# Kernel optimization log

Measured on AMD Instinct MI355X. Metric: run time of the kernel, lower is better.

Reference implementation:

```python
import jax, jax.numpy as jnp
import numpy as np

N = 50000      # nodes
E = 800000     # directed edges
D = 128        # input_dim == hidden_dim
EL = 100000    # edges scored by decoder


def setup_inputs() -> dict:
    key = jax.random.key(0)
    ks = jax.random.split(key, 8)
    s = 1.0 / np.sqrt(D)  # glorot-ish scale
    return {
        "node_feature": jax.random.normal(ks[0], (N, D), jnp.float32),
        "W1": jax.random.normal(ks[1], (D, D), jnp.float32) * s,
        "b1": jnp.zeros((D,), jnp.float32),
        "W2": jax.random.normal(ks[2], (D, D), jnp.float32) * s,
        "b2": jnp.zeros((D,), jnp.float32),
        "W3": jax.random.normal(ks[3], (D, D), jnp.float32) * s,
        "b3": jnp.zeros((D,), jnp.float32),
        "edge_index": jax.random.randint(ks[4], (2, E), 0, N, dtype=jnp.int32),
        "edge_label_index": jax.random.randint(ks[5], (2, EL), 0, N, dtype=jnp.int32),
    }


def _gcn_conv(x, W, b, src, dst, norm, n):
    # x' = D^{-1/2} (A + I) D^{-1/2} (x W) + b   (PyG GCNConv semantics)
    h = x @ W                                   # [N, D]
    msg = h[src] * norm[:, None]                # gather + scale, [E+N, D]
    out = jax.ops.segment_sum(msg, dst, num_segments=n)  # scatter-add
    return out + b


def reference(node_feature, W1, b1, W2, b2, W3, b3, edge_index, edge_label_index):
    n = node_feature.shape[0]
    loop = jnp.arange(n, dtype=edge_index.dtype)
    src = jnp.concatenate([edge_index[0], loop])  # self-loops appended
    dst = jnp.concatenate([edge_index[1], loop])
    # symmetric normalization: deg over destinations (incl. self-loops)
    deg = jax.ops.segment_sum(jnp.ones_like(dst, dtype=node_feature.dtype), dst, num_segments=n)
    dinv = jax.lax.rsqrt(jnp.maximum(deg, 1.0))
    norm = dinv[src] * dinv[dst]                 # [E+N]

    x = jax.nn.relu(_gcn_conv(node_feature, W1, b1, src, dst, norm, n))
    x = jax.nn.relu(_gcn_conv(x, W2, b2, src, dst, norm, n))
    x = _gcn_conv(x, W3, b3, src, dst, norm, n)

    # dot-product edge decoder
    u = x[edge_label_index[0]]
    v = x[edge_label_index[1]]
    return jnp.sum(u * v, axis=-1)               # [EL] logits
```

## Files before the change

kernel.cpp:

```cpp
#include <hip/hip_runtime.h>
#include <hip/hip_bf16.h>
#include <hip/hip_fp16.h>

typedef _Float16 v8h __attribute__((ext_vector_type(8)));
typedef _Float16 v4h __attribute__((ext_vector_type(4)));
typedef float v4f __attribute__((ext_vector_type(4)));

__global__ __launch_bounds__(256) void wswz(const float* __restrict__ W1,
                                            const float* __restrict__ W2,
                                            const float* __restrict__ W3,
                                            __half* __restrict__ wfrag) {
    int o = blockIdx.x * 256 + threadIdx.x;
    int w = o >> 14, r = o & 16383;
    const float* Ws = (w >= 3) ? W3 : ((w == 2) ? W2 : W1);
    float v = Ws[r];
    __half h;
    if (w == 1) {
        __half hv = __float2half_rn(v);
        h = __float2half_rn(v - __half2float(hv));
    } else {
        h = __float2half_rn(v);
    }
    int k = r >> 7, ncol = r & 127;
    int c = ncol >> 4, nl = ncol & 15;
    int s = k >> 5, quad = (k >> 3) & 3, j = k & 7;
    int di = ((c * 4 + s) * 64 + quad * 16 + nl) * 8 + j;
    wfrag[(size_t)w * 16384 + di] = h;
}

__global__ __launch_bounds__(256) void gemm1_mfma(const float* __restrict__ X,
                                                  const __half* __restrict__ wfrag,
                                                  __half* __restrict__ H, int Nrows,
                                                  int degBlocks,
                                                  const int* __restrict__ dst,
                                                  int* __restrict__ cnt,
                                                  int* __restrict__ rank, int E) {
    int tid = threadIdx.x;
    if (blockIdx.x < degBlocks) {
        int base = blockIdx.x * 2048 + tid * 8;
        if (base + 7 < E) {
            int4 d0 = *(const int4*)&dst[base];
            int4 d1 = *(const int4*)&dst[base + 4];
            int r0 = atomicAdd(&cnt[d0.x * 16], 1);
            int r1 = atomicAdd(&cnt[d0.y * 16], 1);
            int r2 = atomicAdd(&cnt[d0.z * 16], 1);
            int r3 = atomicAdd(&cnt[d0.w * 16], 1);
            int r4 = atomicAdd(&cnt[d1.x * 16], 1);
            int r5 = atomicAdd(&cnt[d1.y * 16], 1);
            int r6 = atomicAdd(&cnt[d1.z * 16], 1);
            int r7 = atomicAdd(&cnt[d1.w * 16], 1);
            *(int4*)&rank[base]     = make_int4(r0, r1, r2, r3);
            *(int4*)&rank[base + 4] = make_int4(r4, r5, r6, r7);
        } else {
            for (int e = base; e < E; ++e) rank[e] = atomicAdd(&cnt[dst[e] * 16], 1);
        }
        return;
    }
    int gb = blockIdx.x - degBlocks;
    int rowbase = gb * 64;
    int l = tid & 63;
    int wid = tid >> 6;
    int rb = wid * 16;
    int quad = l >> 4;
    int nn = l & 15;
    int gr = rowbase + rb + nn;
    v8h ah[4], al[4];
    if (gr < Nrows) {
        const float* Xr = &X[(size_t)gr * 128 + quad * 8];
#pragma unroll
        for (int k = 0; k < 4; ++k) {
            float4 f0 = *(const float4*)&Xr[k * 32];
            float4 f1 = *(const float4*)&Xr[k * 32 + 4];
            float ff[8] = {f0.x, f0.y, f0.z, f0.w, f1.x, f1.y, f1.z, f1.w};
            v8h h, lo;
#pragma unroll
            for (int m = 0; m < 8; ++m) {
                _Float16 hv = (_Float16)ff[m];
                h[m] = hv;
                lo[m] = (_Float16)(ff[m] - (float)hv);
            }
            ah[k] = h;
            al[k] = lo;
        }
    } else {
#pragma unroll
        for (int k = 0; k < 4; ++k) {
            v8h z;
#pragma unroll
            for (int m = 0; m < 8; ++m) z[m] = (_Float16)0.f;
            ah[k] = z;
            al[k] = z;
        }
    }
    const v8h* Wh = (const v8h*)wfrag;
    const v8h* Wl = (const v8h*)(wfrag + 16384);
    v4f acc[8] = {};
#pragma unroll
    for (int c = 0; c < 8; ++c) {
        v8h bh0 = Wh[(c * 4 + 0) * 64 + l];
        v8h bh1 = Wh[(c * 4 + 1) * 64 + l];
        v8h bh2 = Wh[(c * 4 + 2) * 64 + l];
        v8h bh3 = Wh[(c * 4 + 3) * 64 + l];
        acc[c] = __builtin_amdgcn_mfma_f32_16x16x32_f16(ah[0], bh0, acc[c], 0, 0, 0);
        acc[c] = __builtin_amdgcn_mfma_f32_16x16x32_f16(ah[1], bh1, acc[c], 0, 0, 0);
        acc[c] = __builtin_amdgcn_mfma_f32_16x16x32_f16(ah[2], bh2, acc[c], 0, 0, 0);
        acc[c] = __builtin_amdgcn_mfma_f32_16x16x32_f16(ah[3], bh3, acc[c], 0, 0, 0);
        acc[c] = __builtin_amdgcn_mfma_f32_16x16x32_f16(al[0], bh0, acc[c], 0, 0, 0);
        acc[c] = __builtin_amdgcn_mfma_f32_16x16x32_f16(al[1], bh1, acc[c], 0, 0, 0);
        acc[c] = __builtin_amdgcn_mfma_f32_16x16x32_f16(al[2], bh2, acc[c], 0, 0, 0);
        acc[c] = __builtin_amdgcn_mfma_f32_16x16x32_f16(al[3], bh3, acc[c], 0, 0, 0);
        v8h bl0 = Wl[(c * 4 + 0) * 64 + l];
        v8h bl1 = Wl[(c * 4 + 1) * 64 + l];
        v8h bl2 = Wl[(c * 4 + 2) * 64 + l];
        v8h bl3 = Wl[(c * 4 + 3) * 64 + l];
        acc[c] = __builtin_amdgcn_mfma_f32_16x16x32_f16(ah[0], bl0, acc[c], 0, 0, 0);
        acc[c] = __builtin_amdgcn_mfma_f32_16x16x32_f16(ah[1], bl1, acc[c], 0, 0, 0);
        acc[c] = __builtin_amdgcn_mfma_f32_16x16x32_f16(ah[2], bl2, acc[c], 0, 0, 0);
        acc[c] = __builtin_amdgcn_mfma_f32_16x16x32_f16(ah[3], bl3, acc[c], 0, 0, 0);
    }
#pragma unroll
    for (int reg = 0; reg < 4; ++reg) {
        int grr = rowbase + rb + quad * 4 + reg;
        if (grr < Nrows) {
#pragma unroll
            for (int c = 0; c < 8; ++c)
                H[(size_t)grr * 128 + c * 16 + nn] = __float2half_rn(acc[c][reg]);
        }
    }
}

__global__ __launch_bounds__(256) void agg_gemm(const __half* __restrict__ Xs,
                                                const float* __restrict__ dinv,
                                                const int* __restrict__ rowptr,
                                                const int* __restrict__ col,
                                                const __half* __restrict__ wfrag,
                                                const float* __restrict__ bias,
                                                __half* __restrict__ Out,
                                                int n, int finalLayer) {
    __shared__ __align__(16) _Float16 y[64][136];
    int tid = threadIdx.x;
    int rowbase = blockIdx.x * 64;
    {
        int sub = tid >> 4;
        int t = (tid & 15) * 8;
        for (int g = 0; g < 4; ++g) {
            int rr = g * 16 + sub;
            int node = rowbase + rr;
            float a[8] = {};
            if (node < n) {
                int beg = rowptr[node], end = rowptr[node + 1];
                int k = beg;
                for (; k + 4 <= end; k += 4) {
                    int s0 = col[k], s1 = col[k + 1], s2 = col[k + 2], s3 = col[k + 3];
                    uint4 r0 = *(const uint4*)&Xs[(size_t)s0 * 128 + t];
                    uint4 r1 = *(const uint4*)&Xs[(size_t)s1 * 128 + t];
                    uint4 r2 = *(const uint4*)&Xs[(size_t)s2 * 128 + t];
                    uint4 r3 = *(const uint4*)&Xs[(size_t)s3 * 128 + t];
                    const __half2* h0 = (const __half2*)&r0;
                    const __half2* h1 = (const __half2*)&r1;
                    const __half2* h2 = (const __half2*)&r2;
                    const __half2* h3 = (const __half2*)&r3;
#pragma unroll
                    for (int m = 0; m < 4; ++m) {
                        float2 f0 = __half22float2(h0[m]);
                        float2 f1 = __half22float2(h1[m]);
                        float2 f2 = __half22float2(h2[m]);
                        float2 f3 = __half22float2(h3[m]);
                        a[2 * m]     += (f0.x + f1.x) + (f2.x + f3.x);
                        a[2 * m + 1] += (f0.y + f1.y) + (f2.y + f3.y);
                    }
                }
                for (; k < end; ++k) {
                    uint4 r0 = *(const uint4*)&Xs[(size_t)col[k] * 128 + t];
                    const __half2* h0 = (const __half2*)&r0;
#pragma unroll
                    for (int m = 0; m < 4; ++m) {
                        float2 f0 = __half22float2(h0[m]);
                        a[2 * m] += f0.x;
                        a[2 * m + 1] += f0.y;
                    }
                }
                float dn = dinv[node];
#pragma unroll
                for (int m = 0; m < 8; ++m) a[m] *= dn;
            }
            v8h yv;
#pragma unroll
            for (int m = 0; m < 8; ++m) yv[m] = (_Float16)a[m];
            *(v8h*)&y[rr][t] = yv;
        }
    }
    __syncthreads();
    int l = tid & 63;
    int wid = tid >> 6;
    int rb = wid * 16;
    int quad = l >> 4;
    int nn = l & 15;
    v8h a0 = *(const v8h*)&y[rb + nn][0 * 32 + quad * 8];
    v8h a1 = *(const v8h*)&y[rb + nn][1 * 32 + quad * 8];
    v8h a2 = *(const v8h*)&y[rb + nn][2 * 32 + quad * 8];
    v8h a3 = *(const v8h*)&y[rb + nn][3 * 32 + quad * 8];
    const v8h* Wf = (const v8h*)wfrag;
    v4f acc[8] = {};
#pragma unroll
    for (int c = 0; c < 8; ++c) {
        v8h b0 = Wf[(c * 4 + 0) * 64 + l];
        v8h b1 = Wf[(c * 4 + 1) * 64 + l];
        v8h b2 = Wf[(c * 4 + 2) * 64 + l];
        v8h b3 = Wf[(c * 4 + 3) * 64 + l];
        acc[c] = __builtin_amdgcn_mfma_f32_16x16x32_f16(a0, b0, acc[c], 0, 0, 0);
        acc[c] = __builtin_amdgcn_mfma_f32_16x16x32_f16(a1, b1, acc[c], 0, 0, 0);
        acc[c] = __builtin_amdgcn_mfma_f32_16x16x32_f16(a2, b2, acc[c], 0, 0, 0);
        acc[c] = __builtin_amdgcn_mfma_f32_16x16x32_f16(a3, b3, acc[c], 0, 0, 0);
    }
#pragma unroll
    for (int reg = 0; reg < 4; ++reg) {
        int gr = rowbase + rb + quad * 4 + reg;
        if (gr < n) {
            float dn = dinv[gr];
#pragma unroll
            for (int c = 0; c < 8; ++c) {
                float z = acc[c][reg] + bias[c * 16 + nn];
                if (!finalLayer) z = fmaxf(z, 0.f) * dn;
                Out[(size_t)gr * 128 + c * 16 + nn] = __float2half_rn(z);
            }
        }
    }
}

__global__ void scanA(const int* __restrict__ cnt, int* __restrict__ tmp,
                      int* __restrict__ bsum, int n) {
    __shared__ int s[256];
    int i = blockIdx.x * 256 + threadIdx.x;
    int v = (i < n) ? (cnt[i * 16] + 1) : 0;
    s[threadIdx.x] = v;
    __syncthreads();
    for (int off = 1; off < 256; off <<= 1) {
        int x = (threadIdx.x >= off) ? s[threadIdx.x - off] : 0;
        __syncthreads();
        s[threadIdx.x] += x;
        __syncthreads();
    }
    if (i < n) tmp[i] = s[threadIdx.x];
    if (threadIdx.x == 255) bsum[blockIdx.x] = s[255];
}

__global__ void scanB(const int* __restrict__ tmp, const int* __restrict__ bsum,
                      const int* __restrict__ cnt, int* __restrict__ rowptr,
                      float* __restrict__ dinv, int* __restrict__ col, int n, int nb) {
    __shared__ int p[256];
    int t = threadIdx.x;
    p[t] = (t < nb) ? bsum[t] : 0;
    __syncthreads();
    for (int off = 1; off < 256; off <<= 1) {
        int x = (t >= off) ? p[t - off] : 0;
        __syncthreads();
        p[t] += x;
        __syncthreads();
    }
    int prefix = (blockIdx.x == 0) ? 0 : p[blockIdx.x - 1];
    int i = blockIdx.x * 256 + t;
    if (i < n) {
        int inc = tmp[i] + prefix;
        rowptr[i + 1] = inc;
        int c1 = cnt[i * 16] + 1;
        dinv[i] = rsqrtf((float)c1);
        col[inc - c1] = i;
        if (i == 0) rowptr[0] = 0;
    }
}

__global__ __launch_bounds__(256) void fill4(const int* __restrict__ src,
                                             const int* __restrict__ dst,
                                             const int* __restrict__ rank,
                                             const int* __restrict__ rowptr,
                                             int* __restrict__ col, int E) {
    int base = blockIdx.x * 1024 + threadIdx.x * 4;
    if (base + 3 < E) {
        int d0 = dst[base], d1 = dst[base + 1], d2 = dst[base + 2], d3 = dst[base + 3];
        int s0 = src[base], s1 = src[base + 1], s2 = src[base + 2], s3 = src[base + 3];
        int r0 = rank[base], r1 = rank[base + 1], r2 = rank[base + 2], r3 = rank[base + 3];
        col[rowptr[d0] + 1 + r0] = s0;
        col[rowptr[d1] + 1 + r1] = s1;
        col[rowptr[d2] + 1 + r2] = s2;
        col[rowptr[d3] + 1 + r3] = s3;
    } else {
        for (int e = base; e < E; ++e)
            col[rowptr[dst[e]] + 1 + rank[e]] = src[e];
    }
}

__global__ __launch_bounds__(256) void agg_h(const __half* __restrict__ H,
                                             const float* __restrict__ dinv,
                                             const int* __restrict__ rowptr,
                                             const int* __restrict__ col,
                                             const float* __restrict__ bias,
                                             __half* __restrict__ out, int n) {
    int node = blockIdx.x * 16 + (threadIdx.x >> 4);
    int t = (threadIdx.x & 15) * 8;
    if (node >= n) return;
    int beg = rowptr[node], end = rowptr[node + 1];
    float a[8] = {};
    int k = beg;
    for (; k + 4 <= end; k += 4) {
        int s0 = col[k], s1 = col[k + 1], s2 = col[k + 2], s3 = col[k + 3];
        float w0 = dinv[s0], w1 = dinv[s1], w2 = dinv[s2], w3 = dinv[s3];
        uint4 r0 = *(const uint4*)&H[(size_t)s0 * 128 + t];
        uint4 r1 = *(const uint4*)&H[(size_t)s1 * 128 + t];
        uint4 r2 = *(const uint4*)&H[(size_t)s2 * 128 + t];
        uint4 r3 = *(const uint4*)&H[(size_t)s3 * 128 + t];
        const __half2* h0 = (const __half2*)&r0;
        const __half2* h1 = (const __half2*)&r1;
        const __half2* h2 = (const __half2*)&r2;
        const __half2* h3 = (const __half2*)&r3;
#pragma unroll
        for (int m = 0; m < 4; ++m) {
            float2 f0 = __half22float2(h0[m]);
            float2 f1 = __half22float2(h1[m]);
            float2 f2 = __half22float2(h2[m]);
            float2 f3 = __half22float2(h3[m]);
            a[2 * m]     += f0.x * w0 + f1.x * w1 + f2.x * w2 + f3.x * w3;
            a[2 * m + 1] += f0.y * w0 + f1.y * w1 + f2.y * w2 + f3.y * w3;
        }
    }
    for (; k < end; ++k) {
        int s0 = col[k];
        float w0 = dinv[s0];
        uint4 r0 = *(const uint4*)&H[(size_t)s0 * 128 + t];
        const __half2* h0 = (const __half2*)&r0;
#pragma unroll
        for (int m = 0; m < 4; ++m) {
            float2 f0 = __half22float2(h0[m]);
            a[2 * m] += f0.x * w0;
            a[2 * m + 1] += f0.y * w0;
        }
    }
    float dn = dinv[node];
    float4 b0 = *(const float4*)&bias[t];
    float4 b1 = *(const float4*)&bias[t + 4];
    float r0 = fmaxf(a[0] * dn + b0.x, 0.f) * dn;
    float r1 = fmaxf(a[1] * dn + b0.y, 0.f) * dn;
    float r2 = fmaxf(a[2] * dn + b0.z, 0.f) * dn;
    float r3 = fmaxf(a[3] * dn + b0.w, 0.f) * dn;
    float r4 = fmaxf(a[4] * dn + b1.x, 0.f) * dn;
    float r5 = fmaxf(a[5] * dn + b1.y, 0.f) * dn;
    float r6 = fmaxf(a[6] * dn + b1.z, 0.f) * dn;
    float r7 = fmaxf(a[7] * dn + b1.w, 0.f) * dn;
    auto pk = [](float x, float y) { __half2 h = __floats2half2_rn(x, y); return *(unsigned int*)&h; };
    uint4 o = make_uint4(pk(r0, r1), pk(r2, r3), pk(r4, r5), pk(r6, r7));
    *(uint4*)&out[(size_t)node * 128 + t] = o;
}

__global__ __launch_bounds__(256) void decoder_h(const __half* __restrict__ X,
                                                 const int* __restrict__ eli,
                                                 float* __restrict__ out, int EL) {
    int e = blockIdx.x * 16 + (threadIdx.x >> 4);
    int lane = threadIdx.x & 15;
    if (e >= EL) return;
    int u = eli[e], v = eli[EL + e];
    uint4 ra = *(const uint4*)&X[(size_t)u * 128 + lane * 8];
    uint4 rb = *(const uint4*)&X[(size_t)v * 128 + lane * 8];
    const __half2* ha = (const __half2*)&ra;
    const __half2* hb = (const __half2*)&rb;
    float d = 0.f;
#pragma unroll
    for (int j = 0; j < 4; ++j) {
        float2 fa = __half22float2(ha[j]);
        float2 fb = __half22float2(hb[j]);
        d += fa.x * fb.x + fa.y * fb.y;
    }
#pragma unroll
    for (int off = 8; off > 0; off >>= 1) d += __shfl_xor(d, off);
    if (lane == 0) out[e] = d;
}

extern "C" void kernel_launch(void* const* d_in, const int* in_sizes, int n_in,
                              void* d_out, int out_size, void* d_ws, size_t ws_size,
                              hipStream_t stream) {
    const float* x0 = (const float*)d_in[0];
    const float* W1 = (const float*)d_in[1];
    const float* b1 = (const float*)d_in[2];
    const float* W2 = (const float*)d_in[3];
    const float* b2 = (const float*)d_in[4];
    const float* W3 = (const float*)d_in[5];
    const float* b3 = (const float*)d_in[6];
    const int* ei   = (const int*)d_in[7];
    const int* eli  = (const int*)d_in[8];
    float* out = (float*)d_out;

    const int D = 128;
    const int N  = in_sizes[0] / D;
    const int E  = in_sizes[7] / 2;
    const int EL = in_sizes[8] / 2;

    const int* src = ei;
    const int* dst = ei + E;

    char* ws = (char*)d_ws;
    size_t off = 0;
    auto alloc = [&](size_t bytes) -> void* {
        off = (off + 255) & ~(size_t)255;
        void* p = ws + off;
        off += bytes;
        return p;
    };
    int*    cnt    = (int*)alloc((size_t)N * 16 * sizeof(int));
    int*    tmp    = (int*)alloc((size_t)N * sizeof(int));
    int*    bsum   = (int*)alloc(256 * sizeof(int));
    int*    rowptr = (int*)alloc((size_t)(N + 1) * sizeof(int));
    float*  dinv   = (float*)alloc((size_t)N * sizeof(float));
    int*    rank   = (int*)alloc((size_t)E * sizeof(int));
    int*    col    = (int*)alloc((size_t)(E + N) * sizeof(int));
    __half* wfrag  = (__half*)alloc((size_t)4 * 16384 * sizeof(__half));
    __half* hbuf   = (__half*)alloc((size_t)N * D * sizeof(__half));
    __half* xbuf   = (__half*)alloc((size_t)N * D * sizeof(__half));
    (void)ws_size;

    hipMemsetAsync(cnt, 0, (size_t)N * 16 * sizeof(int), stream);

    int nbN = (N + 255) / 256;
    int nbE4 = (E + 1023) / 1024;
    int nbE8 = (E + 2047) / 2048;
    int gemmGrid = (N + 63) / 64;
    int fusedGrid = (N + 63) / 64;
    int aggGrid  = (N + 15) / 16;

    wswz<<<256, 256, 0, stream>>>(W1, W2, W3, wfrag);

    gemm1_mfma<<<nbE8 + gemmGrid, 256, 0, stream>>>(x0, wfrag, hbuf, N,
                                                    nbE8, dst, cnt, rank, E);

    scanA<<<nbN, 256, 0, stream>>>(cnt, tmp, bsum, N);
    scanB<<<nbN, 256, 0, stream>>>(tmp, bsum, cnt, rowptr, dinv, col, N, nbN);
    fill4<<<nbE4, 256, 0, stream>>>(src, dst, rank, rowptr, col, E);

    agg_h<<<aggGrid, 256, 0, stream>>>(hbuf, dinv, rowptr, col, b1, xbuf, N);
    agg_gemm<<<fusedGrid, 256, 0, stream>>>(xbuf, dinv, rowptr, col, wfrag + 2 * 16384, b2, hbuf, N, 0);
    agg_gemm<<<fusedGrid, 256, 0, stream>>>(hbuf, dinv, rowptr, col, wfrag + 3 * 16384, b3, xbuf, N, 1);

    decoder_h<<<(EL + 15) / 16, 256, 0, stream>>>(xbuf, eli, out, EL);
}
```

Baseline: 266.5 us.

## Split degree counting from GEMM, compact counters, unroll gathers by eight

The fused degree-count/GEMM launch is split into a standalone deg_rank kernel and a plain gemm1 kernel. The degree counter array drops its 16-int padding, so the memset and scan reads shrink. gemm1 prefetches the next high-part weight fragments while the low-part MFMAs run, and the aggregation loops gain an 8-wide unrolled gather to keep more loads in flight. The risks are losing the overlap between atomics and GEMM that the fused launch gave, and more atomic contention on densely packed counters.

```diff
diff --git a/kernel.cpp b/kernel.cpp
--- a/kernel.cpp
+++ b/kernel.cpp
@@ -28,36 +28,27 @@
     wfrag[(size_t)w * 16384 + di] = h;
 }
 
-__global__ __launch_bounds__(256) void gemm1_mfma(const float* __restrict__ X,
-                                                  const __half* __restrict__ wfrag,
-                                                  __half* __restrict__ H, int Nrows,
-                                                  int degBlocks,
-                                                  const int* __restrict__ dst,
-                                                  int* __restrict__ cnt,
-                                                  int* __restrict__ rank, int E) {
+__global__ __launch_bounds__(256) void deg_rank(const int* __restrict__ dst,
+                                                int* __restrict__ cnt,
+                                                int* __restrict__ rank, int E) {
+    int base = blockIdx.x * 1024 + threadIdx.x * 4;
+    if (base + 3 < E) {
+        int4 d = *(const int4*)&dst[base];
+        int r0 = atomicAdd(&cnt[d.x], 1);
+        int r1 = atomicAdd(&cnt[d.y], 1);
+        int r2 = atomicAdd(&cnt[d.z], 1);
+        int r3 = atomicAdd(&cnt[d.w], 1);
+        *(int4*)&rank[base] = make_int4(r0, r1, r2, r3);
+    } else {
+        for (int e = base; e < E; ++e) rank[e] = atomicAdd(&cnt[dst[e]], 1);
+    }
+}
+
+__global__ __launch_bounds__(256) void gemm1(const float* __restrict__ X,
+                                             const __half* __restrict__ wfrag,
+                                             __half* __restrict__ H, int Nrows) {
     int tid = threadIdx.x;
-    if (blockIdx.x < degBlocks) {
-        int base = blockIdx.x * 2048 + tid * 8;
-        if (base + 7 < E) {
-            int4 d0 = *(const int4*)&dst[base];
-            int4 d1 = *(const int4*)&dst[base + 4];
-            int r0 = atomicAdd(&cnt[d0.x * 16], 1);
-            int r1 = atomicAdd(&cnt[d0.y * 16], 1);
-            int r2 = atomicAdd(&cnt[d0.z * 16], 1);
-            int r3 = atomicAdd(&cnt[d0.w * 16], 1);
-            int r4 = atomicAdd(&cnt[d1.x * 16], 1);
-            int r5 = atomicAdd(&cnt[d1.y * 16], 1);
-            int r6 = atomicAdd(&cnt[d1.z * 16], 1);
-            int r7 = atomicAdd(&cnt[d1.w * 16], 1);
-            *(int4*)&rank[base]     = make_int4(r0, r1, r2, r3);
-            *(int4*)&rank[base + 4] = make_int4(r4, r5, r6, r7);
-        } else {
-            for (int e = base; e < E; ++e) rank[e] = atomicAdd(&cnt[dst[e] * 16], 1);
-        }
-        return;
-    }
-    int gb = blockIdx.x - degBlocks;
-    int rowbase = gb * 64;
+    int rowbase = blockIdx.x * 64;
     int l = tid & 63;
     int wid = tid >> 6;
     int rb = wid * 16;
@@ -95,12 +86,16 @@
     const v8h* Wh = (const v8h*)wfrag;
     const v8h* Wl = (const v8h*)(wfrag + 16384);
     v4f acc[8] = {};
+    v8h bh0 = Wh[0 * 64 + l];
+    v8h bh1 = Wh[1 * 64 + l];
+    v8h bh2 = Wh[2 * 64 + l];
+    v8h bh3 = Wh[3 * 64 + l];
 #pragma unroll
     for (int c = 0; c < 8; ++c) {
-        v8h bh0 = Wh[(c * 4 + 0) * 64 + l];
-        v8h bh1 = Wh[(c * 4 + 1) * 64 + l];
-        v8h bh2 = Wh[(c * 4 + 2) * 64 + l];
-        v8h bh3 = Wh[(c * 4 + 3) * 64 + l];
+        v8h bl0 = Wl[(c * 4 + 0) * 64 + l];
+        v8h bl1 = Wl[(c * 4 + 1) * 64 + l];
+        v8h bl2 = Wl[(c * 4 + 2) * 64 + l];
+        v8h bl3 = Wl[(c * 4 + 3) * 64 + l];
         acc[c] = __builtin_amdgcn_mfma_f32_16x16x32_f16(ah[0], bh0, acc[c], 0, 0, 0);
         acc[c] = __builtin_amdgcn_mfma_f32_16x16x32_f16(ah[1], bh1, acc[c], 0, 0, 0);
         acc[c] = __builtin_amdgcn_mfma_f32_16x16x32_f16(ah[2], bh2, acc[c], 0, 0, 0);
@@ -109,14 +104,18 @@
         acc[c] = __builtin_amdgcn_mfma_f32_16x16x32_f16(al[1], bh1, acc[c], 0, 0, 0);
         acc[c] = __builtin_amdgcn_mfma_f32_16x16x32_f16(al[2], bh2, acc[c], 0, 0, 0);
         acc[c] = __builtin_amdgcn_mfma_f32_16x16x32_f16(al[3], bh3, acc[c], 0, 0, 0);
-        v8h bl0 = Wl[(c * 4 + 0) * 64 + l];
-        v8h bl1 = Wl[(c * 4 + 1) * 64 + l];
-        v8h bl2 = Wl[(c * 4 + 2) * 64 + l];
-        v8h bl3 = Wl[(c * 4 + 3) * 64 + l];
+        v8h nh0, nh1, nh2, nh3;
+        if (c < 7) {
+            nh0 = Wh[((c + 1) * 4 + 0) * 64 + l];
+            nh1 = Wh[((c + 1) * 4 + 1) * 64 + l];
+            nh2 = Wh[((c + 1) * 4 + 2) * 64 + l];
+            nh3 = Wh[((c + 1) * 4 + 3) * 64 + l];
+        }
         acc[c] = __builtin_amdgcn_mfma_f32_16x16x32_f16(ah[0], bl0, acc[c], 0, 0, 0);
         acc[c] = __builtin_amdgcn_mfma_f32_16x16x32_f16(ah[1], bl1, acc[c], 0, 0, 0);
         acc[c] = __builtin_amdgcn_mfma_f32_16x16x32_f16(ah[2], bl2, acc[c], 0, 0, 0);
         acc[c] = __builtin_amdgcn_mfma_f32_16x16x32_f16(ah[3], bl3, acc[c], 0, 0, 0);
+        if (c < 7) { bh0 = nh0; bh1 = nh1; bh2 = nh2; bh3 = nh3; }
     }
 #pragma unroll
     for (int reg = 0; reg < 4; ++reg) {
@@ -150,6 +149,39 @@
             if (node < n) {
                 int beg = rowptr[node], end = rowptr[node + 1];
                 int k = beg;
+                for (; k + 8 <= end; k += 8) {
+                    int s0 = col[k], s1 = col[k + 1], s2 = col[k + 2], s3 = col[k + 3];
+                    int s4 = col[k + 4], s5 = col[k + 5], s6 = col[k + 6], s7 = col[k + 7];
+                    uint4 r0 = *(const uint4*)&Xs[(size_t)s0 * 128 + t];
+                    uint4 r1 = *(const uint4*)&Xs[(size_t)s1 * 128 + t];
+                    uint4 r2 = *(const uint4*)&Xs[(size_t)s2 * 128 + t];
+                    uint4 r3 = *(const uint4*)&Xs[(size_t)s3 * 128 + t];
+                    uint4 r4 = *(const uint4*)&Xs[(size_t)s4 * 128 + t];
+                    uint4 r5 = *(const uint4*)&Xs[(size_t)s5 * 128 + t];
+                    uint4 r6 = *(const uint4*)&Xs[(size_t)s6 * 128 + t];
+                    uint4 r7 = *(const uint4*)&Xs[(size_t)s7 * 128 + t];
+                    const __half2* h0 = (const __half2*)&r0;
+                    const __half2* h1 = (const __half2*)&r1;
+                    const __half2* h2 = (const __half2*)&r2;
+                    const __half2* h3 = (const __half2*)&r3;
+                    const __half2* h4 = (const __half2*)&r4;
+                    const __half2* h5 = (const __half2*)&r5;
+                    const __half2* h6 = (const __half2*)&r6;
+                    const __half2* h7 = (const __half2*)&r7;
+#pragma unroll
+                    for (int m = 0; m < 4; ++m) {
+                        float2 f0 = __half22float2(h0[m]);
+                        float2 f1 = __half22float2(h1[m]);
+                        float2 f2 = __half22float2(h2[m]);
+                        float2 f3 = __half22float2(h3[m]);
+                        float2 f4 = __half22float2(h4[m]);
+                        float2 f5 = __half22float2(h5[m]);
+                        float2 f6 = __half22float2(h6[m]);
+                        float2 f7 = __half22float2(h7[m]);
+                        a[2 * m]     += ((f0.x + f1.x) + (f2.x + f3.x)) + ((f4.x + f5.x) + (f6.x + f7.x));
+                        a[2 * m + 1] += ((f0.y + f1.y) + (f2.y + f3.y)) + ((f4.y + f5.y) + (f6.y + f7.y));
+                    }
+                }
                 for (; k + 4 <= end; k += 4) {
                     int s0 = col[k], s1 = col[k + 1], s2 = col[k + 2], s3 = col[k + 3];
                     uint4 r0 = *(const uint4*)&Xs[(size_t)s0 * 128 + t];
@@ -232,7 +264,7 @@
                       int* __restrict__ bsum, int n) {
     __shared__ int s[256];
     int i = blockIdx.x * 256 + threadIdx.x;
-    int v = (i < n) ? (cnt[i * 16] + 1) : 0;
+    int v = (i < n) ? (cnt[i] + 1) : 0;
     s[threadIdx.x] = v;
     __syncthreads();
     for (int off = 1; off < 256; off <<= 1) {
@@ -263,7 +295,7 @@
     if (i < n) {
         int inc = tmp[i] + prefix;
         rowptr[i + 1] = inc;
-        int c1 = cnt[i * 16] + 1;
+        int c1 = cnt[i] + 1;
         dinv[i] = rsqrtf((float)c1);
         col[inc - c1] = i;
         if (i == 0) rowptr[0] = 0;
@@ -302,6 +334,43 @@
     int beg = rowptr[node], end = rowptr[node + 1];
     float a[8] = {};
     int k = beg;
+    for (; k + 8 <= end; k += 8) {
+        int s0 = col[k], s1 = col[k + 1], s2 = col[k + 2], s3 = col[k + 3];
+        int s4 = col[k + 4], s5 = col[k + 5], s6 = col[k + 6], s7 = col[k + 7];
+        float w0 = dinv[s0], w1 = dinv[s1], w2 = dinv[s2], w3 = dinv[s3];
+        float w4 = dinv[s4], w5 = dinv[s5], w6 = dinv[s6], w7 = dinv[s7];
+        uint4 r0 = *(const uint4*)&H[(size_t)s0 * 128 + t];
+        uint4 r1 = *(const uint4*)&H[(size_t)s1 * 128 + t];
+        uint4 r2 = *(const uint4*)&H[(size_t)s2 * 128 + t];
+        uint4 r3 = *(const uint4*)&H[(size_t)s3 * 128 + t];
+        uint4 r4 = *(const uint4*)&H[(size_t)s4 * 128 + t];
+        uint4 r5 = *(const uint4*)&H[(size_t)s5 * 128 + t];
+        uint4 r6 = *(const uint4*)&H[(size_t)s6 * 128 + t];
+        uint4 r7 = *(const uint4*)&H[(size_t)s7 * 128 + t];
+        const __half2* h0 = (const __half2*)&r0;
+        const __half2* h1 = (const __half2*)&r1;
+        const __half2* h2 = (const __half2*)&r2;
+        const __half2* h3 = (const __half2*)&r3;
+        const __half2* h4 = (const __half2*)&r4;
+        const __half2* h5 = (const __half2*)&r5;
+        const __half2* h6 = (const __half2*)&r6;
+        const __half2* h7 = (const __half2*)&r7;
+#pragma unroll
+        for (int m = 0; m < 4; ++m) {
+            float2 f0 = __half22float2(h0[m]);
+            float2 f1 = __half22float2(h1[m]);
+            float2 f2 = __half22float2(h2[m]);
+            float2 f3 = __half22float2(h3[m]);
+            float2 f4 = __half22float2(h4[m]);
+            float2 f5 = __half22float2(h5[m]);
+            float2 f6 = __half22float2(h6[m]);
+            float2 f7 = __half22float2(h7[m]);
+            a[2 * m]     += (f0.x * w0 + f1.x * w1 + f2.x * w2 + f3.x * w3)
+                          + (f4.x * w4 + f5.x * w5 + f6.x * w6 + f7.x * w7);
+            a[2 * m + 1] += (f0.y * w0 + f1.y * w1 + f2.y * w2 + f3.y * w3)
+                          + (f4.y * w4 + f5.y * w5 + f6.y * w6 + f7.y * w7);
+        }
+    }
     for (; k + 4 <= end; k += 4) {
         int s0 = col[k], s1 = col[k + 1], s2 = col[k + 2], s3 = col[k + 3];
         float w0 = dinv[s0], w1 = dinv[s1], w2 = dinv[s2], w3 = dinv[s3];
@@ -404,7 +473,7 @@
         off += bytes;
         return p;
     };
-    int*    cnt    = (int*)alloc((size_t)N * 16 * sizeof(int));
+    int*    cnt    = (int*)alloc((size_t)N * sizeof(int));
     int*    tmp    = (int*)alloc((size_t)N * sizeof(int));
     int*    bsum   = (int*)alloc(256 * sizeof(int));
     int*    rowptr = (int*)alloc((size_t)(N + 1) * sizeof(int));
@@ -416,19 +485,18 @@
     __half* xbuf   = (__half*)alloc((size_t)N * D * sizeof(__half));
     (void)ws_size;
 
-    hipMemsetAsync(cnt, 0, (size_t)N * 16 * sizeof(int), stream);
+    hipMemsetAsync(cnt, 0, (size_t)N * sizeof(int), stream);
 
     int nbN = (N + 255) / 256;
     int nbE4 = (E + 1023) / 1024;
-    int nbE8 = (E + 2047) / 2048;
     int gemmGrid = (N + 63) / 64;
     int fusedGrid = (N + 63) / 64;
     int aggGrid  = (N + 15) / 16;
 
     wswz<<<256, 256, 0, stream>>>(W1, W2, W3, wfrag);
 
-    gemm1_mfma<<<nbE8 + gemmGrid, 256, 0, stream>>>(x0, wfrag, hbuf, N,
-                                                    nbE8, dst, cnt, rank, E);
+    deg_rank<<<nbE4, 256, 0, stream>>>(dst, cnt, rank, E);
+    gemm1<<<gemmGrid, 256, 0, stream>>>(x0, wfrag, hbuf, N);
 
     scanA<<<nbN, 256, 0, stream>>>(cnt, tmp, bsum, N);
     scanB<<<nbN, 256, 0, stream>>>(tmp, bsum, cnt, rowptr, dinv, col, N, nbN);
```

Measured after the change: 275.1 us. 3.2% more time.
